# Optimization experiments

Hardware: AMD Instinct MI355X
Metric: run time of the kernel (lower is better)

Reference implementation:

```python
import jax, jax.numpy as jnp
import numpy as np


def setup_inputs() -> dict:
    key = jax.random.key(0)
    k1, k2 = jax.random.split(key)
    B, C, L, K = 16, 64, 4096, 1024
    x = jax.random.normal(k1, (B, C, L), dtype=jnp.float32)
    codebook = jax.random.normal(k2, (K, C), dtype=jnp.float32)
    return {"x": x, "codebook": codebook}


def reference(x, codebook):
    # x: (B, C, L), codebook: (K, C)
    B, C, L = x.shape
    xt = jnp.transpose(x, (0, 2, 1))  # (B, L, C)

    # Squared Euclidean distances (argmin is invariant to the sqrt in torch.cdist)
    x2 = jnp.sum(xt * xt, axis=-1, keepdims=True)            # (B, L, 1)
    w2 = jnp.sum(codebook * codebook, axis=-1)               # (K,)
    xw = jnp.einsum("blc,kc->blk", xt, codebook)             # (B, L, K)
    d2 = x2 - 2.0 * xw + w2                                   # (B, L, K)
    min_encoding_indices = jnp.argmin(d2, axis=-1)            # (B, L)

    quant = codebook[min_encoding_indices]                    # (B, L, C)

    commitment_loss = jnp.mean((jax.lax.stop_gradient(quant) - xt) ** 2)
    codebook_loss = jnp.mean((quant - jax.lax.stop_gradient(xt)) ** 2)

    # Straight-through estimator
    quant_out = xt + jax.lax.stop_gradient(quant - xt)        # (B, L, C)
    quant_out = jnp.transpose(quant_out, (0, 2, 1))           # (B, C, L)

    return quant_out, codebook_loss, commitment_loss, min_encoding_indices
```

## Files before the change

### kernel.cpp

```cpp
#include <hip/hip_runtime.h>

#define BATCH 16
#define CH    64
#define LEN   4096
#define NCODE 1024
#define NPTS  (BATCH * LEN)
#define NPART 512
#define UNITB 24576

typedef float float2v __attribute__((ext_vector_type(2)));
typedef float float4v __attribute__((ext_vector_type(4)));
typedef short short8  __attribute__((ext_vector_type(8)));
typedef float f32x16  __attribute__((ext_vector_type(16)));
typedef unsigned int uint32;

__device__ __forceinline__ unsigned short f2bf(float f) {
    uint32 u = __builtin_bit_cast(uint32, f);
    u += 0x7fffu + ((u >> 16) & 1u);
    return (unsigned short)(u >> 16);
}
__device__ __forceinline__ float bf2f(unsigned short h) {
    uint32 u = ((uint32)h) << 16;
    return __builtin_bit_cast(float, u);
}

__global__ __launch_bounds__(256) void vq_prep(const float* __restrict__ cb,
                                               short* __restrict__ cbf2,
                                               float* __restrict__ w2tab) {
    __shared__ float tile[64][65];
    __shared__ float s2p[4][64];
    const int k0 = blockIdx.x * 64;
    const int t  = threadIdx.x;
#pragma unroll
    for (int it = 0; it < 4; ++it) {
        int idx = it * 256 + t, row = idx >> 4, q = idx & 15;
        *(float4v*)&tile[row][q * 4] =
            *(const float4v*)&cb[(size_t)(k0 + row) * CH + q * 4];
    }
    __syncthreads();

    const int j  = t & 63;
    const int cq = t >> 6;
    const int k  = k0 + j, T = k >> 5, row = k & 31;
    const int Tp = (T < 16) ? (T * 2) : ((T - 16) * 2 + 1);
    float s2 = 0.f;
#pragma unroll
    for (int cc = 0; cc < 16; ++cc) {
        float xv = tile[j][cq * 16 + cc];
        s2 = fmaf(xv, xv, s2);
        unsigned short h1 = f2bf(xv); float f1 = bf2f(h1);
        float r1 = xv - f1;
        unsigned short h2 = f2bf(r1); float f2 = bf2f(h2);
        float r2 = r1 - f2;
        unsigned short h3 = f2bf(r2);
        int g = cc >> 3, i = cc & 7;
        int lane = g * 32 + row;
        size_t base = ((size_t)Tp * 12 + cq * 3) * 512 + lane * 8 + i;
        cbf2[base]        = (short)h1;
        cbf2[base + 512]  = (short)h2;
        cbf2[base + 1024] = (short)h3;
    }
    s2p[cq][j] = s2;
    __syncthreads();
    if (t < 64) {
        float s2t = ((s2p[0][t] + s2p[1][t]) + (s2p[2][t] + s2p[3][t]));
        int kk = k0 + t, TT = kk >> 5, rr = kk & 31;
        int hi = (rr >> 2) & 1, r = (rr & 3) + 4 * (rr >> 3);
        w2tab[((size_t)TT * 2 + hi) * 16 + r] = s2t;
    }
}

__device__ __forceinline__ void epi(const f32x16& acc, int Tg, int g,
                                    float& bestc, int& bestk,
                                    const float* w2s) {
    const float4v* wt = (const float4v*)(w2s + ((size_t)Tg * 2 + g) * 16);
    float4v w0 = wt[0], w1 = wt[1], w2v = wt[2], w3 = wt[3];
    float wr[16] = {w0.x, w0.y, w0.z, w0.w, w1.x, w1.y, w1.z, w1.w,
                    w2v.x, w2v.y, w2v.z, w2v.w, w3.x, w3.y, w3.z, w3.w};
    int kbase = Tg * 32 + 4 * g;
#pragma unroll
    for (int r = 0; r < 16; ++r) {
        float cost = fmaf(-2.0f, acc[r], wr[r]);
        int kg = kbase + (r & 3) + 8 * (r >> 2);
        if (cost < bestc) { bestc = cost; bestk = kg; }
    }
}

__global__ void __launch_bounds__(512)
__attribute__((amdgpu_waves_per_eu(4, 4)))
vq_argmin(const float*  __restrict__ x,
          const float*  __restrict__ cb,
          const short*  __restrict__ cbf2,
          const float*  __restrict__ w2tab,
          float*        __restrict__ quant,
          float*        __restrict__ idx_out,
          double*       __restrict__ partial) {
    __shared__ __attribute__((aligned(16))) char  ring[3 * UNITB];
    __shared__ __attribute__((aligned(16))) float w2s[NCODE];

    float*  smc  = (float*)ring;
    int*    smk  = (int*)(ring + 1024);
    int*    fidx = (int*)(ring + 2048);
    double* sds  = (double*)(ring + 2560);

    const int t   = threadIdx.x;
    const int l   = t & 63;
    const int w   = __builtin_amdgcn_readfirstlane(t >> 6);
    const int h2  = w >> 2;
    const int ptl = (w & 3) * 32 + (l & 31);
    const int g   = l >> 5;
    const int p0  = blockIdx.x * 128;
    const int b   = p0 >> 12;
    const int l0  = p0 & (LEN - 1);

    float* xs = (float*)ring;

#pragma unroll
    for (int it = 0; it < 4; ++it) {
        int fi = it * 512 + t, c = fi >> 5, p4 = fi & 31;
        *(float4v*)&xs[c * 128 + 4 * p4] =
            *(const float4v*)&x[((size_t)b * CH + c) * LEN + l0 + 4 * p4];
    }
    w2s[t]       = w2tab[t];
    w2s[t + 512] = w2tab[t + 512];
    __syncthreads();

    short8 B1[4], B2[4], B3[4];
    float x2p = 0.f;
#pragma unroll
    for (int s = 0; s < 4; ++s) {
#pragma unroll
        for (int i = 0; i < 8; ++i) {
            int c = s * 16 + g * 8 + i;
            float xv = xs[c * 128 + ptl];
            x2p = fmaf(xv, xv, x2p);
            unsigned short h1v = f2bf(xv); float f1 = bf2f(h1v);
            float r1 = xv - f1;
            unsigned short h2v = f2bf(r1); float f2 = bf2f(h2v);
            float r2 = r1 - f2;
            unsigned short h3v = f2bf(r2);
            B1[s][i] = (short)h1v; B2[s][i] = (short)h2v; B3[s][i] = (short)h3v;
        }
    }
    const float x2 = x2p + __shfl_xor(x2p, 32, 64);
    __syncthreads();

    const float4v* gsrc = (const float4v*)cbf2;

    float4v sA0, sA1, sA2, sB0, sB1, sB2;
    sA0 = gsrc[t]; sA1 = gsrc[512 + t]; sA2 = gsrc[1024 + t];
    {
        float4v* d = (float4v*)ring;
        d[t] = sA0; d[512 + t] = sA1; d[1024 + t] = sA2;
    }
    sA0 = gsrc[1536 + t]; sA1 = gsrc[2048 + t]; sA2 = gsrc[2560 + t];
    asm volatile("s_waitcnt lgkmcnt(0)" ::: "memory");
    __builtin_amdgcn_s_barrier();
    asm volatile("" ::: "memory");

    float bestc = 3.4e38f;
    int   bestk = 0;

    auto STEP = [&](int tt, float4v& cu0, float4v& cu1, float4v& cu2,
                    float4v& nx0, float4v& nx1, float4v& nx2) {
        if (tt + 2 < 16) {
            const float4v* gs = gsrc + (size_t)(tt + 2) * 1536;
            nx0 = gs[t]; nx1 = gs[512 + t]; nx2 = gs[1024 + t];
        }
        const short* bp = (const short*)&ring[(tt % 3) * UNITB] + h2 * 6144;
        f32x16 acc = {0.f,0.f,0.f,0.f,0.f,0.f,0.f,0.f,
                      0.f,0.f,0.f,0.f,0.f,0.f,0.f,0.f};
        __builtin_amdgcn_s_setprio(1);
#pragma unroll
        for (int s = 0; s < 4; ++s) {
            const short* fb = bp + (s * 3) * 512 + l * 8;
            short8 A1 = *(const short8*)(fb);
            short8 A2 = *(const short8*)(fb + 512);
            short8 A3 = *(const short8*)(fb + 1024);
            acc = __builtin_amdgcn_mfma_f32_32x32x16_bf16(A1, B1[s], acc, 0, 0, 0);
            acc = __builtin_amdgcn_mfma_f32_32x32x16_bf16(A1, B2[s], acc, 0, 0, 0);
            acc = __builtin_amdgcn_mfma_f32_32x32x16_bf16(A2, B1[s], acc, 0, 0, 0);
            acc = __builtin_amdgcn_mfma_f32_32x32x16_bf16(A1, B3[s], acc, 0, 0, 0);
            acc = __builtin_amdgcn_mfma_f32_32x32x16_bf16(A3, B1[s], acc, 0, 0, 0);
            acc = __builtin_amdgcn_mfma_f32_32x32x16_bf16(A2, B2[s], acc, 0, 0, 0);
        }
        __builtin_amdgcn_s_setprio(0);
        epi(acc, h2 * 16 + tt, g, bestc, bestk, w2s);
        if (tt + 1 < 16) {
            float4v* d = (float4v*)&ring[((tt + 1) % 3) * UNITB];
            d[t] = cu0; d[512 + t] = cu1; d[1024 + t] = cu2;
        }
        asm volatile("s_waitcnt lgkmcnt(0)" ::: "memory");
        __builtin_amdgcn_s_barrier();
        asm volatile("" ::: "memory");
    };

    for (int tp = 0; tp < 8; ++tp) {
        STEP(2 * tp,     sA0, sA1, sA2, sB0, sB1, sB2);
        STEP(2 * tp + 1, sB0, sB1, sB2, sA0, sA1, sA2);
    }

    {
        float ob = __shfl_xor(bestc, 32, 64);
        int   ok = __shfl_xor(bestk, 32, 64);
        if (ob < bestc || (ob == bestc && ok < bestk)) { bestc = ob; bestk = ok; }
    }
    __syncthreads();
    if (l < 32) { smc[w * 32 + l] = bestc; smk[w * 32 + l] = bestk; }
    __syncthreads();
    if (w < 4 && l < 32) {
        float ob = smc[(w + 4) * 32 + l];
        int   ok = smk[(w + 4) * 32 + l];
        if (ob < bestc || (ob == bestc && ok < bestk)) { bestc = ob; bestk = ok; }
        idx_out[p0 + w * 32 + l] = (float)bestk;
        fidx[w * 32 + l] = bestk;
        sds[w * 32 + l] = (double)x2 + (double)bestc;
    }
    __syncthreads();

    {
        const int pt = t & 127;
        const int cq = t >> 7;
        const int k  = fidx[pt];
        const float4v* src = (const float4v*)(cb + (size_t)k * CH + cq * 16);
        float4v v0 = src[0], v1 = src[1], v2 = src[2], v3 = src[3];
        float vr[16] = {v0.x, v0.y, v0.z, v0.w, v1.x, v1.y, v1.z, v1.w,
                        v2.x, v2.y, v2.z, v2.w, v3.x, v3.y, v3.z, v3.w};
#pragma unroll
        for (int j = 0; j < 16; ++j) {
            int c = cq * 16 + j;
            quant[((size_t)b * CH + c) * LEN + l0 + pt] = vr[j];
        }
    }

    if (t == 0) {
        double s = 0.0;
        for (int i = 0; i < 128; ++i) s += sds[i];
        partial[blockIdx.x] = s;
    }
}

__global__ __launch_bounds__(256) void vq_loss(const double* __restrict__ partial,
                                               float*        __restrict__ losses) {
    __shared__ double sred[256];
    double v = 0.0;
#pragma unroll
    for (int i = 0; i < NPART / 256; ++i) v += partial[threadIdx.x + 256 * i];
    sred[threadIdx.x] = v;
    __syncthreads();
    for (int s = 128; s > 0; s >>= 1) {
        if (threadIdx.x < s) sred[threadIdx.x] += sred[threadIdx.x + s];
        __syncthreads();
    }
    if (threadIdx.x == 0) {
        float loss = (float)(sred[0] / (double)((size_t)NPTS * CH));
        losses[0] = loss;
        losses[1] = loss;
    }
}

extern "C" void kernel_launch(void* const* d_in, const int* in_sizes, int n_in,
                              void* d_out, int out_size, void* d_ws, size_t ws_size,
                              hipStream_t stream) {
    const float* x  = (const float*)d_in[0];
    const float* cb = (const float*)d_in[1];
    float* out = (float*)d_out;

    float* quant_out = out;
    float* losses    = out + (size_t)BATCH * CH * LEN;
    float* idx_out   = losses + 2;

    double* partial = (double*)d_ws;
    float*  w2tab   = (float*)((char*)d_ws + 4096);
    short*  cbf2    = (short*)((char*)d_ws + 16384);

    vq_prep<<<16, 256, 0, stream>>>(cb, cbf2, w2tab);
    vq_argmin<<<NPTS / 128, 512, 0, stream>>>(x, cb, cbf2, w2tab,
                                              quant_out, idx_out, partial);
    vq_loss<<<1, 256, 0, stream>>>(partial, losses);
}
```

Before: 60.11 us.

## Stream codebook tiles into LDS with direct global-to-LDS async loads

Replaces the register-staged codebook prefetch (global load to VGPRs, then ds_write into a 3-slot LDS ring) with global_load_lds instructions that write straight into the ring slot two steps ahead. Synchronisation now uses vmcnt waits plus barriers instead of lgkmcnt. This is meant to free the staging VGPRs and drop the LDS write instructions from the MFMA loop, so copy and compute overlap better. The risk is subtle ordering problems, because the async writes land in LDS while other waves may still be reading the slot being overwritten.

```diff
diff --git a/kernel.cpp b/kernel.cpp
--- a/kernel.cpp
+++ b/kernel.cpp
@@ -22,6 +22,13 @@
 __device__ __forceinline__ float bf2f(unsigned short h) {
     uint32 u = ((uint32)h) << 16;
     return __builtin_bit_cast(float, u);
+}
+
+__device__ __forceinline__ void gll16(const void* g, void* l) {
+    __builtin_amdgcn_global_load_lds(
+        (const __attribute__((address_space(1))) void*)(g),
+        (__attribute__((address_space(3))) void*)(l),
+        16, 0, 0);
 }
 
 __global__ __launch_bounds__(256) void vq_prep(const float* __restrict__ cb,
@@ -145,28 +152,17 @@
     const float x2 = x2p + __shfl_xor(x2p, 32, 64);
     __syncthreads();
 
-    const float4v* gsrc = (const float4v*)cbf2;
-
-    float4v sA0, sA1, sA2, sB0, sB1, sB2;
-    sA0 = gsrc[t]; sA1 = gsrc[512 + t]; sA2 = gsrc[1024 + t];
-    {
-        float4v* d = (float4v*)ring;
-        d[t] = sA0; d[512 + t] = sA1; d[1024 + t] = sA2;
-    }
-    sA0 = gsrc[1536 + t]; sA1 = gsrc[2048 + t]; sA2 = gsrc[2560 + t];
-    asm volatile("s_waitcnt lgkmcnt(0)" ::: "memory");
-    __builtin_amdgcn_s_barrier();
-    asm volatile("" ::: "memory");
+    auto issue_unit = [&](int u) {
+        const char* gu = (const char*)cbf2 + (size_t)u * UNITB + (size_t)(l * 16);
+        char*       lu = ring + (u % 3) * UNITB + w * 1024;
+#pragma unroll
+        for (int j = 0; j < 3; ++j)
+            gll16(gu + (w * 1024 + j * 8192), lu + j * 8192);
+    };
 
     float bestc = 3.4e38f;
     int   bestk = 0;
-
-    auto STEP = [&](int tt, float4v& cu0, float4v& cu1, float4v& cu2,
-                    float4v& nx0, float4v& nx1, float4v& nx2) {
-        if (tt + 2 < 16) {
-            const float4v* gs = gsrc + (size_t)(tt + 2) * 1536;
-            nx0 = gs[t]; nx1 = gs[512 + t]; nx2 = gs[1024 + t];
-        }
+    auto COMPUTE = [&](int tt) {
         const short* bp = (const short*)&ring[(tt % 3) * UNITB] + h2 * 6144;
         f32x16 acc = {0.f,0.f,0.f,0.f,0.f,0.f,0.f,0.f,
                       0.f,0.f,0.f,0.f,0.f,0.f,0.f,0.f};
@@ -186,19 +182,26 @@
         }
         __builtin_amdgcn_s_setprio(0);
         epi(acc, h2 * 16 + tt, g, bestc, bestk, w2s);
-        if (tt + 1 < 16) {
-            float4v* d = (float4v*)&ring[((tt + 1) % 3) * UNITB];
-            d[t] = cu0; d[512 + t] = cu1; d[1024 + t] = cu2;
-        }
-        asm volatile("s_waitcnt lgkmcnt(0)" ::: "memory");
+    };
+
+    issue_unit(0);
+    issue_unit(1);
+    asm volatile("s_waitcnt vmcnt(3)" ::: "memory");
+    __builtin_amdgcn_s_barrier();
+    asm volatile("" ::: "memory");
+
+    for (int tt = 0; tt < 14; ++tt) {
+        issue_unit(tt + 2);
+        COMPUTE(tt);
+        asm volatile("s_waitcnt vmcnt(3)" ::: "memory");
         __builtin_amdgcn_s_barrier();
         asm volatile("" ::: "memory");
-    };
-
-    for (int tp = 0; tp < 8; ++tp) {
-        STEP(2 * tp,     sA0, sA1, sA2, sB0, sB1, sB2);
-        STEP(2 * tp + 1, sB0, sB1, sB2, sA0, sA1, sA2);
-    }
+    }
+    COMPUTE(14);
+    asm volatile("s_waitcnt vmcnt(0)" ::: "memory");
+    __builtin_amdgcn_s_barrier();
+    asm volatile("" ::: "memory");
+    COMPUTE(15);
 
     {
         float ob = __shfl_xor(bestc, 32, 64);
```

New measurement: 58.78 us. 1.02x faster.
